# Kernel tuning notes

Measured on AMD Instinct MI355X. Metric: run time of the kernel, lower is better.

The kernel has to match this reference:

```python
import jax, jax.numpy as jnp
import numpy as np
import math

B, T, E, H = 64, 256, 1024, 16
HD = E // H  # 64
EPS = 1e-5


def layernorm(x, g, b):
    mu = jnp.mean(x, axis=-1, keepdims=True)
    var = jnp.mean(jnp.square(x - mu), axis=-1, keepdims=True)
    return (x - mu) * jax.lax.rsqrt(var + EPS) * g + b


def setup_inputs() -> dict:
    key = jax.random.key(0)
    ks = jax.random.split(key, 10)
    s = 0.02
    return {
        "x": jax.random.normal(ks[0], (B, T, E), dtype=jnp.float32),
        "ln1_g": jnp.ones((E,), jnp.float32),
        "ln1_b": jnp.zeros((E,), jnp.float32),
        "wk": jax.random.normal(ks[1], (H, E, HD), jnp.float32) * s,
        "wq": jax.random.normal(ks[2], (H, E, HD), jnp.float32) * s,
        "wv": jax.random.normal(ks[3], (H, E, HD), jnp.float32) * s,
        "w_proj": jax.random.normal(ks[4], (E, E), jnp.float32) * s,
        "b_proj": jnp.zeros((E,), jnp.float32),
        "ln2_g": jnp.ones((E,), jnp.float32),
        "ln2_b": jnp.zeros((E,), jnp.float32),
        "w1": jax.random.normal(ks[5], (E, E), jnp.float32) * s,
        "b1": jnp.zeros((E,), jnp.float32),
        "w2": jax.random.normal(ks[6], (E, E), jnp.float32) * s,
        "b2": jnp.zeros((E,), jnp.float32),
    }


def reference(x, ln1_g, ln1_b, wk, wq, wv, w_proj, b_proj, ln2_g, ln2_b, w1, b1, w2, b2):
    # --- multi-head causal attention on LN1(x) ---
    h = layernorm(x, ln1_g, ln1_b)
    k = jnp.einsum('bte,hed->bhtd', h, wk)
    q = jnp.einsum('bte,hed->bhtd', h, wq)
    v = jnp.einsum('bte,hed->bhtd', h, wv)
    # NOTE: original computes k @ q^T (K.Q^T), not the standard Q.K^T -- kept faithful
    scores = jnp.einsum('bhtd,bhsd->bhts', k, q) / math.sqrt(HD)
    mask = jnp.tril(jnp.ones((T, T), dtype=bool))
    scores = jnp.where(mask, scores, -jnp.inf)
    attn_w = jax.nn.softmax(scores, axis=-1)  # dropout = identity in eval
    attn = jnp.einsum('bhts,bhsd->bhtd', attn_w, v)
    attn = attn.transpose(0, 2, 1, 3).reshape(B, T, E)  # concat heads
    x = x + attn @ w_proj + b_proj
    # --- feed-forward on LN2(x) ---
    h2 = layernorm(x, ln2_g, ln2_b)
    ff = jax.nn.relu(h2 @ w1 + b1) @ w2 + b2
    return x + ff
```

## Files before the change

kernel.cpp:

```cpp
#include <hip/hip_runtime.h>

typedef unsigned int u32;
typedef unsigned short u16;
typedef __attribute__((ext_vector_type(8))) short bf16x8;
typedef __attribute__((ext_vector_type(4))) float f32x4;

#define GLOBAL_AS __attribute__((address_space(1)))
#define LDS_AS    __attribute__((address_space(3)))

#define B_   64
#define T_   256
#define E_   1024
#define H_   16
#define HD_  64
#define NTOK (B_*T_)
#define K_   1024
#define LNEPS 1e-5f

__device__ __forceinline__ u16 f2bf(float f){
  u32 x = __float_as_uint(f);
  u32 r = x + 0x7fffu + ((x >> 16) & 1u);
  return (u16)(r >> 16);
}
__device__ __forceinline__ u16 f2bf_trunc(float f){
  return (u16)(__float_as_uint(f) >> 16);
}
__device__ __forceinline__ u32 pack2(float a, float b){
  return (u32)f2bf(a) | ((u32)f2bf(b) << 16);
}

__device__ __forceinline__ void gload16(const u16* g, u16* l){
  __builtin_amdgcn_global_load_lds((const GLOBAL_AS void*)g, (LDS_AS void*)l, 16, 0, 0);
}

__global__ __launch_bounds__(256) void ln_bf16_kernel(
    const float* __restrict__ x, const float* __restrict__ g,
    const float* __restrict__ b, u16* __restrict__ o)
{
  int lane  = threadIdx.x & 63;
  int token = (blockIdx.x << 2) + (threadIdx.x >> 6);
  const float4* xr = (const float4*)(x + (size_t)token * E_);
  float4 v[4];
  float s = 0.f, ss = 0.f;
  #pragma unroll
  for (int i = 0; i < 4; ++i){
    v[i] = xr[lane + 64 * i];
    s += v[i].x + v[i].y + v[i].z + v[i].w;
    ss = fmaf(v[i].x, v[i].x, fmaf(v[i].y, v[i].y,
         fmaf(v[i].z, v[i].z, fmaf(v[i].w, v[i].w, ss))));
  }
  #pragma unroll
  for (int off = 32; off > 0; off >>= 1){
    s  += __shfl_xor(s,  off);
    ss += __shfl_xor(ss, off);
  }
  float mu   = s * (1.f / E_);
  float var  = ss * (1.f / E_) - mu * mu;
  float rstd = rsqrtf(var + LNEPS);
  const float4* gr = (const float4*)g;
  const float4* br = (const float4*)b;
  uint2* orow = (uint2*)(o + (size_t)token * E_);
  #pragma unroll
  for (int i = 0; i < 4; ++i){
    float4 gg = gr[lane + 64 * i], bb = br[lane + 64 * i];
    float y0 = (v[i].x - mu) * rstd * gg.x + bb.x;
    float y1 = (v[i].y - mu) * rstd * gg.y + bb.y;
    float y2 = (v[i].z - mu) * rstd * gg.z + bb.z;
    float y3 = (v[i].w - mu) * rstd * gg.w + bb.w;
    orow[lane + 64 * i] = make_uint2(pack2(y0, y1), pack2(y2, y3));
  }
}

__global__ __launch_bounds__(256) void convq_kernel(
    const float* __restrict__ wk, const float* __restrict__ wq,
    const float* __restrict__ wv, u16* __restrict__ o)
{
  __shared__ float tile[64 * 68];
  const int zh = blockIdx.x, z = zh >> 4, h = zh & 15;
  const int k0 = blockIdx.y << 6;
  const float* w = (z == 0 ? wk : z == 1 ? wq : wv) + (size_t)h * (E_ * HD_);
  const int t = threadIdx.x;
  {
    int kr = t >> 2, d0 = (t & 3) << 4;
    const float4* src = (const float4*)(w + (size_t)(k0 + kr) * HD_ + d0);
    #pragma unroll
    for (int i = 0; i < 4; ++i)
      *(float4*)(tile + kr * 68 + d0 + 4 * i) = src[i];
  }
  __syncthreads();
  {
    const size_t nb32 = (size_t)zh * 32 + (k0 >> 5);
    #pragma unroll
    for (int u = 0; u < 2; ++u) {
      int cid = t * 2 + u;
      int dd = cid >> 3, kc = cid & 7;
      u32 wd[4];
      #pragma unroll
      for (int e2 = 0; e2 < 4; ++e2)
        wd[e2] = pack2(tile[(kc * 8 + 2 * e2) * 68 + dd],
                       tile[(kc * 8 + 2 * e2 + 1) * 68 + dd]);
      u16* dst = o + (nb32 + (kc >> 2)) * 2048 + (size_t)(dd >> 4) * 512
                   + (size_t)(((kc & 3) << 4) + (dd & 15)) * 8;
      *(uint4*)dst = make_uint4(wd[0], wd[1], wd[2], wd[3]);
    }
  }
}

__global__ __launch_bounds__(256) void convt_kernel(
    const float* __restrict__ w, u16* __restrict__ o)
{
  __shared__ float tile[64 * 68];
  const int n0 = blockIdx.x << 6, k0 = blockIdx.y << 6;
  const int t = threadIdx.x;
  {
    int kr = t >> 2, nn = (t & 3) << 4;
    const float4* src = (const float4*)(w + (size_t)(k0 + kr) * E_ + n0 + nn);
    #pragma unroll
    for (int i = 0; i < 4; ++i)
      *(float4*)(tile + kr * 68 + nn + 4 * i) = src[i];
  }
  __syncthreads();
  {
    const size_t nb32 = (size_t)(n0 >> 6) * 32 + (k0 >> 5);
    #pragma unroll
    for (int u = 0; u < 2; ++u) {
      int cid = t * 2 + u;
      int dd = cid >> 3, kc = cid & 7;
      u32 wd[4];
      #pragma unroll
      for (int e2 = 0; e2 < 4; ++e2)
        wd[e2] = pack2(tile[(kc * 8 + 2 * e2) * 68 + dd],
                       tile[(kc * 8 + 2 * e2 + 1) * 68 + dd]);
      u16* dst = o + (nb32 + (kc >> 2)) * 2048 + (size_t)(dd >> 4) * 512
                   + (size_t)(((kc & 3) << 4) + (dd & 15)) * 8;
      *(uint4*)dst = make_uint4(wd[0], wd[1], wd[2], wd[3]);
    }
  }
}

#define MF4(I, AV, BV)                                                               \
  acc[I][0] = __builtin_amdgcn_mfma_f32_16x16x32_bf16(AV, BV[0], acc[I][0], 0, 0, 0);\
  acc[I][1] = __builtin_amdgcn_mfma_f32_16x16x32_bf16(AV, BV[1], acc[I][1], 0, 0, 0);\
  acc[I][2] = __builtin_amdgcn_mfma_f32_16x16x32_bf16(AV, BV[2], acc[I][2], 0, 0, 0);\
  acc[I][3] = __builtin_amdgcn_mfma_f32_16x16x32_bf16(AV, BV[3], acc[I][3], 0, 0, 0);

#define BLOADS(BV, SS) {                                                      \
    const u16* bp_ = Bp + (size_t)(SS) * 2048;                                \
    BV[0] = *(const bf16x8*)(bp_);                                            \
    BV[1] = *(const bf16x8*)(bp_ + 512);                                      \
    BV[2] = *(const bf16x8*)(bp_ + 1024);                                     \
    BV[3] = *(const bf16x8*)(bp_ + 1536);                                     \
  }

#define MSLICE2(SLOT, NSLOT, KA, DO_STAGE, DO_NXT, DO_BL, BS, ACUR, ATMP, ANXT, BV, BNV, VM) { \
    const u16* As_ = lds + (SLOT) * 4096;                                     \
          \
    ATMP[0] = *(const bf16x8*)(As_ + aoffb + 1024);                           \
    ATMP[1] = *(const bf16x8*)(As_ + aoffb + 1536);                           \
    if (DO_STAGE) {                                                           \
      u16* d_ = lds + (((SLOT) + 3) & 3) * 4096;                              \
      gload16(Ag0 + (KA), d_ + tid * 8);                                      \
      gload16(Ag1 + (KA), d_ + 2048 + tid * 8);                               \
    }                                                                         \
    __builtin_amdgcn_s_setprio(1);                                            \
    MF4(0, ACUR[0], BV) MF4(1, ACUR[1], BV)                                   \
    __builtin_amdgcn_s_setprio(0);                                            \
             \
    if (DO_NXT) {                                                             \
      const u16* An_ = lds + (NSLOT) * 4096;                                  \
      ANXT[0] = *(const bf16x8*)(An_ + aoffb);                                \
      ANXT[1] = *(const bf16x8*)(An_ + aoffb + 512);                          \
    }                                                                         \
    __builtin_amdgcn_s_setprio(1);                                            \
    MF4(2, ATMP[0], BV) MF4(3, ATMP[1], BV)                                   \
    __builtin_amdgcn_s_setprio(0);                                            \
    if (DO_BL) { BLOADS(BNV, BS) }                                            \
    VM;                                                                       \
    __builtin_amdgcn_s_barrier();                                             \
    __builtin_amdgcn_sched_barrier(0);                                        \
    asm volatile("" ::: "memory");                                            \
  }

#define VM10 asm volatile("s_waitcnt vmcnt(10)" ::: "memory")
#define VM8  asm volatile("s_waitcnt vmcnt(8)"  ::: "memory")
#define VM4  asm volatile("s_waitcnt vmcnt(4)"  ::: "memory")

template<int MODE>
__global__ __launch_bounds__(256, 3) void mgemm_kernel(
    const u16* __restrict__ A, const u16* __restrict__ Bt,
    const float* __restrict__ bias, const float* __restrict__ resid,
    float* __restrict__ Cf, u16* __restrict__ Cb, u16* __restrict__ Cb2)
{
  __shared__ __align__(16) u16 lds[16384];

  const int tid = threadIdx.x, lane = tid & 63, wid = tid >> 6;
  const int wm = wid >> 1, wn = wid & 1;
  const int l15 = lane & 15, quad = lane >> 4;

  const int b = (int)blockIdx.x;
  const int xcd = b & 7, ib = b >> 3;
  const int mloc = ib & 15, ntile = ib >> 4;
  const int row0 = (xcd * 16 + mloc) << 7;
  const int col0 = ntile << 7;

  const int sc   = (tid & 7) ^ ((tid >> 3) & 7);
  const int srow = 2 * (tid >> 3) + (sc >> 2);
  const int skof = (sc & 3) << 3;
  const u16* Ag0 = A + (size_t)(row0 + srow) * K_ + skof;
  const u16* Ag1 = Ag0 + (size_t)64 * K_;

  const int rhalf = l15 >> 1;
  const int cph   = ((((l15 & 1) << 2) | quad) ^ rhalf);
  const int aoffb = wm * 2048 + rhalf * 64 + cph * 8;

  const u16* Bp = Bt + (size_t)((col0 >> 6) + wn) * 65536 + lane * 8;

  f32x4 acc[4][4];
  #pragma unroll
  for (int i = 0; i < 4; ++i)
    #pragma unroll
    for (int j = 0; j < 4; ++j)
      acc[i][j] = (f32x4){0.f, 0.f, 0.f, 0.f};

  bf16x8 aA[2], aB[2], aT[2], bE[4], bO[4];

  #pragma unroll
  for (int t3 = 0; t3 < 3; ++t3) {
    u16* d_ = lds + t3 * 4096;
    gload16(Ag0 + t3 * 32, d_ + tid * 8);
    gload16(Ag1 + t3 * 32, d_ + 2048 + tid * 8);
  }
  BLOADS(bE, 0)
  BLOADS(bO, 1)
  asm volatile("s_waitcnt vmcnt(10)" ::: "memory");
  __builtin_amdgcn_s_barrier();
  __builtin_amdgcn_sched_barrier(0);
  asm volatile("" ::: "memory");

  aA[0] = *(const bf16x8*)(lds + aoffb);
  aA[1] = *(const bf16x8*)(lds + aoffb + 512);

  #pragma unroll 1
  for (int s = 0; s < 28; s += 2) {
    MSLICE2(s & 3, (s + 1) & 3, (s + 3) * 32, 1, 1, 1, s + 2, aA, aT, aB, bE, bE, VM10)
    MSLICE2((s + 1) & 3, (s + 2) & 3, (s + 4) * 32, 1, 1, 1, s + 3, aB, aT, aA, bO, bO, VM10)
  }
  MSLICE2(0, 1, 31 * 32, 1, 1, 1, 30, aA, aT, aB, bE, bE, VM10)
  MSLICE2(1, 2, 0,       0, 1, 1, 31, aB, aT, aA, bO, bO, VM8 )
  MSLICE2(2, 3, 0,       0, 1, 0, 0,  aA, aT, aB, bE, bE, VM4 )
  MSLICE2(3, 0, 0,       0, 0, 0, 0,  aB, aT, aA, bO, bO, (void)0)

  if (MODE == 1 || MODE == 3) {
    const int rbase = row0 + wm * 64;
    #pragma unroll
    for (int j = 0; j < 4; ++j) {
      const int n = col0 + wn * 64 + j * 16 + l15;
      const float bn = bias[n];
      #pragma unroll
      for (int i = 0; i < 4; ++i)
        #pragma unroll
        for (int r = 0; r < 4; ++r) {
          const int row = rbase + i * 16 + quad * 4 + r;
          const size_t idx = (size_t)row * E_ + n;
          float v = acc[i][j][r] + bn;
          if (MODE == 1) Cf[idx] = v + resid[idx];
          else           Cf[idx] = v + Cf[idx];
        }
    }
    return;
  }

  u16* ep = lds + wid * 4096;
  const int nb0 = col0 + wn * 64;

  if (MODE == 2) {
    #pragma unroll
    for (int j = 0; j < 4; ++j) {
      const float bn = bias[nb0 + j * 16 + l15];
      #pragma unroll
      for (int i = 0; i < 4; ++i)
        #pragma unroll
        for (int r = 0; r < 4; ++r)
          ep[(i*16 + quad*4 + r) * 64 + j*16 + l15] =
              f2bf(fmaxf(acc[i][j][r] + bn, 0.f));
    }
    const int rbase = row0 + wm * 64;
    #pragma unroll
    for (int it = 0; it < 8; ++it) {
      const int tl = it * 8 + (lane >> 3), c = lane & 7;
      uint4 v = *(const uint4*)(ep + tl * 64 + c * 8);
      *(uint4*)(Cb + (size_t)(rbase + tl) * E_ + nb0 + c * 8) = v;
    }
    return;
  }

  const int z = nb0 >> 10, hh = (nb0 >> 6) & 15;
  const int rows0 = row0 + wm * 64;
  const int bb = rows0 >> 8, tb = rows0 & 255;
  if (z < 2) {
    #pragma unroll
    for (int i = 0; i < 4; ++i)
      #pragma unroll
      for (int j = 0; j < 4; ++j)
        #pragma unroll
        for (int r = 0; r < 4; ++r)
          ep[(i*16 + quad*4 + r) * 64 + j*16 + l15] = f2bf(acc[i][j][r]);
    u16* out = (z == 0 ? Cb : Cb2) + ((size_t)(bb * H_ + hh) * T_ + tb) * HD_;
    #pragma unroll
    for (int it = 0; it < 8; ++it) {
      const int tl = it * 8 + (lane >> 3), c = lane & 7;
      uint4 v = *(const uint4*)(ep + tl * 64 + c * 8);
      *(uint4*)(out + (size_t)tl * HD_ + c * 8) = v;
    }
  } else {
    #pragma unroll
    for (int i = 0; i < 4; ++i)
      #pragma unroll
      for (int j = 0; j < 4; ++j)
        #pragma unroll
        for (int r = 0; r < 4; ++r) {
          const int tl = i*16 + quad*4 + r, d = j*16 + l15;
          const int cs = (tl >> 3) ^ (d & 7);
          ep[d * 64 + cs * 8 + (tl & 7)] = f2bf(acc[i][j][r]);
        }
    u16* out = (u16*)Cf + ((size_t)(bb * H_ + hh) * HD_) * T_;
    #pragma unroll
    for (int it = 0; it < 8; ++it) {
      const int d = it * 8 + (lane >> 3), c = lane & 7;
      const int cs = c ^ (d & 7);
      uint4 v = *(const uint4*)(ep + d * 64 + cs * 8);
      *(uint4*)(out + (size_t)d * T_ + tb + c * 8) = v;
    }
  }
}

__global__ __launch_bounds__(256) void fattn_kernel(
    const u16* __restrict__ kk_, const u16* __restrict__ qq_,
    const u16* __restrict__ vt_, u16* __restrict__ out)
{
  __shared__ __align__(16) u16 Pb[4][64 * 72];
  const int tid = threadIdx.x, lane = tid & 63, wv = tid >> 6;
  const int bh = blockIdx.x * 4 + wv;
  const int tblk = blockIdx.y;
  const int l15 = lane & 15, quad = lane >> 4;
  const u16* kb  = kk_ + (size_t)bh * (T_ * HD_);
  const u16* qb  = qq_ + (size_t)bh * (T_ * HD_);
  const u16* vtb = vt_ + (size_t)bh * (HD_ * T_);
  u16* Pw = Pb[wv];

  bf16x8 kf[4][2];
  #pragma unroll
  for (int i = 0; i < 4; ++i)
    #pragma unroll
    for (int c = 0; c < 2; ++c)
      kf[i][c] = *(const bf16x8*)(kb + (size_t)(tblk*64 + i*16 + l15) * HD_ + c*32 + quad*8);

  f32x4 o[4][4];
  float mrow[4][4], lrow[4][4];
  #pragma unroll
  for (int i = 0; i < 4; ++i) {
    #pragma unroll
    for (int j = 0; j < 4; ++j) o[i][j] = (f32x4){0.f, 0.f, 0.f, 0.f};
    #pragma unroll
    for (int r = 0; r < 4; ++r) { mrow[i][r] = -1e30f; lrow[i][r] = 0.f; }
  }

  for (int sb = 0; sb <= tblk; ++sb) {
    f32x4 S[4][4];
    #pragma unroll
    for (int j = 0; j < 4; ++j) {
      bf16x8 qf0 = *(const bf16x8*)(qb + (size_t)(sb*64 + j*16 + l15) * HD_ +      quad*8);
      bf16x8 qf1 = *(const bf16x8*)(qb + (size_t)(sb*64 + j*16 + l15) * HD_ + 32 + quad*8);
      #pragma unroll
      for (int i = 0; i < 4; ++i) {
        f32x4 t0 = __builtin_amdgcn_mfma_f32_16x16x32_bf16(kf[i][0], qf0,
                       (f32x4){0.f,0.f,0.f,0.f}, 0, 0, 0);
        S[i][j] = __builtin_amdgcn_mfma_f32_16x16x32_bf16(kf[i][1], qf1, t0, 0, 0, 0);
      }
    }
    #pragma unroll
    for (int i = 0; i < 4; ++i)
      #pragma unroll
      for (int j = 0; j < 4; ++j)
        #pragma unroll
        for (int r = 0; r < 4; ++r) {
          float val = S[i][j][r] * 0.125f;
          if (sb == tblk) {
            int tl = i*16 + quad*4 + r, sl = j*16 + l15;
            if (sl > tl) val = -1e30f;
          }
          S[i][j][r] = val;
        }
    #pragma unroll
    for (int i = 0; i < 4; ++i)
      #pragma unroll
      for (int r = 0; r < 4; ++r) {
        float mx = fmaxf(fmaxf(S[i][0][r], S[i][1][r]), fmaxf(S[i][2][r], S[i][3][r]));
        #pragma unroll
        for (int msk = 1; msk < 16; msk <<= 1) mx = fmaxf(mx, __shfl_xor(mx, msk));
        float mn = fmaxf(mrow[i][r], mx);
        float al = __expf(mrow[i][r] - mn);
        mrow[i][r] = mn;
        float sm = 0.f;
        #pragma unroll
        for (int j = 0; j < 4; ++j) {
          float p = __expf(S[i][j][r] - mn);
          S[i][j][r] = p;
          sm += p;
        }
        #pragma unroll
        for (int msk = 1; msk < 16; msk <<= 1) sm += __shfl_xor(sm, msk);
        lrow[i][r] = lrow[i][r] * al + sm;
        #pragma unroll
        for (int jd = 0; jd < 4; ++jd) o[i][jd][r] *= al;
      }
    #pragma unroll
    for (int i = 0; i < 4; ++i)
      #pragma unroll
      for (int j = 0; j < 4; ++j)
        #pragma unroll
        for (int r = 0; r < 4; ++r)
          Pw[(i*16 + quad*4 + r) * 72 + j*16 + l15] = f2bf_trunc(S[i][j][r]);
    bf16x8 pf[4][2];
    #pragma unroll
    for (int i = 0; i < 4; ++i)
      #pragma unroll
      for (int c = 0; c < 2; ++c)
        pf[i][c] = *(const bf16x8*)(Pw + (i*16 + l15) * 72 + c*32 + quad*8);
    #pragma unroll
    for (int jd = 0; jd < 4; ++jd) {
      bf16x8 vf0 = *(const bf16x8*)(vtb + (size_t)(jd*16 + l15) * T_ + sb*64 +      quad*8);
      bf16x8 vf1 = *(const bf16x8*)(vtb + (size_t)(jd*16 + l15) * T_ + sb*64 + 32 + quad*8);
      #pragma unroll
      for (int i = 0; i < 4; ++i) {
        f32x4 t0 = __builtin_amdgcn_mfma_f32_16x16x32_bf16(pf[i][0], vf0, o[i][jd], 0, 0, 0);
        o[i][jd] = __builtin_amdgcn_mfma_f32_16x16x32_bf16(pf[i][1], vf1, t0, 0, 0, 0);
      }
    }
  }

  #pragma unroll
  for (int i = 0; i < 4; ++i)
    #pragma unroll
    for (int r = 0; r < 4; ++r) {
      float inv = 1.0f / lrow[i][r];
      #pragma unroll
      for (int jd = 0; jd < 4; ++jd)
        Pw[(i*16 + quad*4 + r) * 72 + jd*16 + l15] = f2bf(o[i][jd][r] * inv);
    }
  {
    const int b = bh >> 4, h = bh & 15;
    const uint4* pr = (const uint4*)(Pw + lane * 72);
    uint4* og = (uint4*)(out + ((size_t)(b * T_ + tblk*64 + lane)) * E_ + h * HD_);
    #pragma unroll
    for (int k = 0; k < 8; ++k) og[k] = pr[k];
  }
}

extern "C" void kernel_launch(void* const* d_in, const int* in_sizes, int n_in,
                              void* d_out, int out_size, void* d_ws, size_t ws_size,
                              hipStream_t stream) {
  const float* x     = (const float*)d_in[0];
  const float* ln1g  = (const float*)d_in[1];
  const float* ln1b  = (const float*)d_in[2];
  const float* wk    = (const float*)d_in[3];
  const float* wq    = (const float*)d_in[4];
  const float* wv    = (const float*)d_in[5];
  const float* wproj = (const float*)d_in[6];
  const float* bproj = (const float*)d_in[7];
  const float* ln2g  = (const float*)d_in[8];
  const float* ln2b  = (const float*)d_in[9];
  const float* w1    = (const float*)d_in[10];
  const float* b1    = (const float*)d_in[11];
  const float* w2    = (const float*)d_in[12];
  const float* b2    = (const float*)d_in[13];
  float* outp = (float*)d_out;

  char* ws = (char*)d_ws;
  const size_t MB = 1024 * 1024;
  u16* wqkvT  = (u16*)(ws);
  u16* wprojT = (u16*)(ws + 6 * MB);
  u16* w1T    = (u16*)(ws + 8 * MB);
  u16* w2T    = (u16*)(ws + 10 * MB);
  u16* hb     = (u16*)(ws + 16 * MB);
  u16* kbuf   = (u16*)(ws + 48 * MB);
  u16* qbuf   = (u16*)(ws + 80 * MB);
  u16* vtbuf  = (u16*)d_out;

  convq_kernel<<<dim3(48, 16), 256, 0, stream>>>(wk, wq, wv, wqkvT);
  convt_kernel<<<dim3(16, 16), 256, 0, stream>>>(wproj, wprojT);
  convt_kernel<<<dim3(16, 16), 256, 0, stream>>>(w1, w1T);
  convt_kernel<<<dim3(16, 16), 256, 0, stream>>>(w2, w2T);

  ln_bf16_kernel<<<NTOK/4, 256, 0, stream>>>(x, ln1g, ln1b, hb);
  mgemm_kernel<0><<<3072, 256, 0, stream>>>(
      hb, wqkvT, nullptr, nullptr, (float*)vtbuf, kbuf, qbuf);
  fattn_kernel<<<dim3(B_*H_/4, 4), 256, 0, stream>>>(kbuf, qbuf, vtbuf, hb);
  mgemm_kernel<1><<<1024, 256, 0, stream>>>(
      hb, wprojT, bproj, x, outp, nullptr, nullptr);
  ln_bf16_kernel<<<NTOK/4, 256, 0, stream>>>(outp, ln2g, ln2b, kbuf);
  mgemm_kernel<2><<<1024, 256, 0, stream>>>(
      kbuf, w1T, b1, nullptr, nullptr, qbuf, nullptr);
  mgemm_kernel<3><<<1024, 256, 0, stream>>>(
      qbuf, w2T, b2, nullptr, outp, nullptr, nullptr);
}
```

Before: 513.8 us.

## Remap attention blocks per head, prefetch Q/V fragments, fuse weight-transpose launches

The attention kernel now assigns one workgroup per (batch, head), with each of its four waves handling one query-time block. Before, each workgroup mixed four heads for a single time block. Q fragments for the next block are loaded in registers ahead of use, and V fragments are loaded before the softmax so their latency overlaps the softmax work. MFMA sections are wrapped in s_setprio. Separately, the three weight transpose/convert launches are merged into one grid with a z dimension to cut launch overhead. Waves within a workgroup now have very unequal causal work (1 to 4 blocks). Register pressure also rises, and launch_bounds(256,1) is set to allow it.

```diff
diff --git a/kernel.cpp b/kernel.cpp
--- a/kernel.cpp
+++ b/kernel.cpp
@@ -106,10 +106,15 @@
   }
 }
 
-__global__ __launch_bounds__(256) void convt_kernel(
-    const float* __restrict__ w, u16* __restrict__ o)
+__global__ __launch_bounds__(256) void convt3_kernel(
+    const float* __restrict__ wp, const float* __restrict__ w1,
+    const float* __restrict__ w2, u16* __restrict__ op,
+    u16* __restrict__ o1, u16* __restrict__ o2)
 {
   __shared__ float tile[64 * 68];
+  const int z = blockIdx.z;
+  const float* w = (z == 0 ? wp : z == 1 ? w1 : w2);
+  u16* o = (z == 0 ? op : z == 1 ? o1 : o2);
   const int n0 = blockIdx.x << 6, k0 = blockIdx.y << 6;
   const int t = threadIdx.x;
   {
@@ -334,14 +339,14 @@
   }
 }
 
-__global__ __launch_bounds__(256) void fattn_kernel(
+__global__ __launch_bounds__(256, 1) void fattn_kernel(
     const u16* __restrict__ kk_, const u16* __restrict__ qq_,
     const u16* __restrict__ vt_, u16* __restrict__ out)
 {
   __shared__ __align__(16) u16 Pb[4][64 * 72];
   const int tid = threadIdx.x, lane = tid & 63, wv = tid >> 6;
-  const int bh = blockIdx.x * 4 + wv;
-  const int tblk = blockIdx.y;
+  const int bh = blockIdx.x;
+  const int tblk = wv;
   const int l15 = lane & 15, quad = lane >> 4;
   const u16* kb  = kk_ + (size_t)bh * (T_ * HD_);
   const u16* qb  = qq_ + (size_t)bh * (T_ * HD_);
@@ -355,6 +360,13 @@
     for (int c = 0; c < 2; ++c)
       kf[i][c] = *(const bf16x8*)(kb + (size_t)(tblk*64 + i*16 + l15) * HD_ + c*32 + quad*8);
 
+  bf16x8 qf[4][2];
+  #pragma unroll
+  for (int j = 0; j < 4; ++j)
+    #pragma unroll
+    for (int c = 0; c < 2; ++c)
+      qf[j][c] = *(const bf16x8*)(qb + (size_t)(j*16 + l15) * HD_ + c*32 + quad*8);
+
   f32x4 o[4][4];
   float mrow[4][4], lrow[4][4];
   #pragma unroll
@@ -367,17 +379,29 @@
 
   for (int sb = 0; sb <= tblk; ++sb) {
     f32x4 S[4][4];
-    #pragma unroll
-    for (int j = 0; j < 4; ++j) {
-      bf16x8 qf0 = *(const bf16x8*)(qb + (size_t)(sb*64 + j*16 + l15) * HD_ +      quad*8);
-      bf16x8 qf1 = *(const bf16x8*)(qb + (size_t)(sb*64 + j*16 + l15) * HD_ + 32 + quad*8);
+    __builtin_amdgcn_s_setprio(1);
+    #pragma unroll
+    for (int j = 0; j < 4; ++j)
       #pragma unroll
       for (int i = 0; i < 4; ++i) {
-        f32x4 t0 = __builtin_amdgcn_mfma_f32_16x16x32_bf16(kf[i][0], qf0,
+        f32x4 t0 = __builtin_amdgcn_mfma_f32_16x16x32_bf16(kf[i][0], qf[j][0],
                        (f32x4){0.f,0.f,0.f,0.f}, 0, 0, 0);
-        S[i][j] = __builtin_amdgcn_mfma_f32_16x16x32_bf16(kf[i][1], qf1, t0, 0, 0, 0);
+        S[i][j] = __builtin_amdgcn_mfma_f32_16x16x32_bf16(kf[i][1], qf[j][1], t0, 0, 0, 0);
       }
-    }
+    __builtin_amdgcn_s_setprio(0);
+    if (sb < tblk) {
+      #pragma unroll
+      for (int j = 0; j < 4; ++j)
+        #pragma unroll
+        for (int c = 0; c < 2; ++c)
+          qf[j][c] = *(const bf16x8*)(qb + (size_t)((sb+1)*64 + j*16 + l15) * HD_ + c*32 + quad*8);
+    }
+    bf16x8 vf[4][2];
+    #pragma unroll
+    for (int jd = 0; jd < 4; ++jd)
+      #pragma unroll
+      for (int c = 0; c < 2; ++c)
+        vf[jd][c] = *(const bf16x8*)(vtb + (size_t)(jd*16 + l15) * T_ + sb*64 + c*32 + quad*8);
     #pragma unroll
     for (int i = 0; i < 4; ++i)
       #pragma unroll
@@ -427,16 +451,15 @@
       #pragma unroll
       for (int c = 0; c < 2; ++c)
         pf[i][c] = *(const bf16x8*)(Pw + (i*16 + l15) * 72 + c*32 + quad*8);
-    #pragma unroll
-    for (int jd = 0; jd < 4; ++jd) {
-      bf16x8 vf0 = *(const bf16x8*)(vtb + (size_t)(jd*16 + l15) * T_ + sb*64 +      quad*8);
-      bf16x8 vf1 = *(const bf16x8*)(vtb + (size_t)(jd*16 + l15) * T_ + sb*64 + 32 + quad*8);
+    __builtin_amdgcn_s_setprio(1);
+    #pragma unroll
+    for (int jd = 0; jd < 4; ++jd)
       #pragma unroll
       for (int i = 0; i < 4; ++i) {
-        f32x4 t0 = __builtin_amdgcn_mfma_f32_16x16x32_bf16(pf[i][0], vf0, o[i][jd], 0, 0, 0);
-        o[i][jd] = __builtin_amdgcn_mfma_f32_16x16x32_bf16(pf[i][1], vf1, t0, 0, 0, 0);
+        f32x4 t0 = __builtin_amdgcn_mfma_f32_16x16x32_bf16(pf[i][0], vf[jd][0], o[i][jd], 0, 0, 0);
+        o[i][jd] = __builtin_amdgcn_mfma_f32_16x16x32_bf16(pf[i][1], vf[jd][1], t0, 0, 0, 0);
       }
-    }
+    __builtin_amdgcn_s_setprio(0);
   }
 
   #pragma unroll
@@ -488,14 +511,12 @@
   u16* vtbuf  = (u16*)d_out;
 
   convq_kernel<<<dim3(48, 16), 256, 0, stream>>>(wk, wq, wv, wqkvT);
-  convt_kernel<<<dim3(16, 16), 256, 0, stream>>>(wproj, wprojT);
-  convt_kernel<<<dim3(16, 16), 256, 0, stream>>>(w1, w1T);
-  convt_kernel<<<dim3(16, 16), 256, 0, stream>>>(w2, w2T);
+  convt3_kernel<<<dim3(16, 16, 3), 256, 0, stream>>>(wproj, w1, w2, wprojT, w1T, w2T);
 
   ln_bf16_kernel<<<NTOK/4, 256, 0, stream>>>(x, ln1g, ln1b, hb);
   mgemm_kernel<0><<<3072, 256, 0, stream>>>(
       hb, wqkvT, nullptr, nullptr, (float*)vtbuf, kbuf, qbuf);
-  fattn_kernel<<<dim3(B_*H_/4, 4), 256, 0, stream>>>(kbuf, qbuf, vtbuf, hb);
+  fattn_kernel<<<B_*H_, 256, 0, stream>>>(kbuf, qbuf, vtbuf, hb);
   mgemm_kernel<1><<<1024, 256, 0, stream>>>(
       hb, wprojT, bproj, x, outp, nullptr, nullptr);
   ln_bf16_kernel<<<NTOK/4, 256, 0, stream>>>(outp, ln2g, ln2b, kbuf);
```

New measurement: 526.0 us. 1.02x slower.
